# Kernel tuning notes

Measured on AMD Instinct MI355X. Metric: run time of the kernel, lower is better.

Reference implementation:

```python
import jax, jax.numpy as jnp
import numpy as np
import math
from jax import lax

KSIZE = 3
STRIDE = 1
RATE = 2
FUSE_K = 3
SCALE = 10.0
FUSE = True


def extract_image_patches(img, kernel, stride=1):
    # Faithful port of the torch helper (incl. pad_row applied to width).
    bsz, c, h, w = img.shape
    h2 = math.ceil(h / stride)
    w2 = math.ceil(w / stride)
    pad_row = (h2 - 1) * stride + kernel - h
    pad_col = (w2 - 1) * stride + kernel - w
    x = jnp.pad(img, ((0, 0), (0, 0),
                      (pad_col // 2, pad_col - pad_col // 2),
                      (pad_row // 2, pad_row - pad_row // 2)))
    H, W = x.shape[2], x.shape[3]
    nh = (H - kernel) // stride + 1
    nw = (W - kernel) // stride + 1
    parts = [x[:, :, ki:ki + (nh - 1) * stride + 1:stride,
                     kj:kj + (nw - 1) * stride + 1:stride]
             for ki in range(kernel) for kj in range(kernel)]
    p = jnp.stack(parts, axis=1)  # [b, k*k, c, nh, nw] -> flatten order (ki,kj,c)
    return p.reshape(bsz, kernel * kernel * c, nh, nw)


def setup_inputs() -> dict:
    key = jax.random.key(0)
    k1, k2 = jax.random.split(key)
    f = jax.random.normal(k1, (2, 64, 128, 128), dtype=jnp.float32)
    b = jax.random.normal(k2, (2, 64, 128, 128), dtype=jnp.float32)
    mask = jnp.zeros((2, 1, 128, 128), dtype=jnp.float32)
    return {"f": f, "b": b, "mask": mask}


def reference(f, b, mask):
    kernel = RATE * 2
    bs, cs, hs, ws = f.shape
    # raw background patches at stride=rate with kernel=2*rate
    raw_w = extract_image_patches(b, kernel, RATE * STRIDE)
    raw_w = raw_w.reshape(bs, -1, kernel, kernel, cs).transpose(0, 1, 4, 2, 3)  # [bs,L,cs,K,K]
    # nearest-neighbor downsample by rate (torch nearest: src = dst*rate)
    f_ds = f[:, :, ::RATE, ::RATE]
    b_ds = b[:, :, ::RATE, ::RATE]
    mask_ds = mask[:, :, ::RATE, ::RATE]
    ihs, iws = b_ds.shape[2], b_ds.shape[3]
    L = ihs * iws
    # ksize x ksize matching patches
    w = extract_image_patches(b_ds, KSIZE, STRIDE)
    w = w.reshape(bs, -1, KSIZE, KSIZE, cs).transpose(0, 1, 4, 2, 3)  # [bs,L,cs,3,3]
    # mask patches -> per-patch validity mm [L]
    m = extract_image_patches(mask_ds, KSIZE, STRIDE)
    m = m.reshape(bs, -1, KSIZE, KSIZE, 1).transpose(0, 2, 3, 4, 1)[0]  # [3,3,1,L]
    mm = (jnp.mean(m, axis=(0, 1, 2)) == 0.0).astype(f.dtype)  # [L]
    fuse_weight = jnp.eye(FUSE_K, dtype=f.dtype).reshape(1, 1, FUSE_K, FUSE_K)

    def per_sample(xi, wi, raw_wi):
        # xi [cs,ihs,iws], wi [L,cs,3,3], raw_wi [L,cs,K,K]
        norm = jnp.sqrt(jnp.sum(wi * wi, axis=(1, 2, 3)))
        wi_normed = wi / jnp.minimum(norm, 1e-4)[:, None, None, None]  # clamp(max=1e-4), faithful
        yi = lax.conv_general_dilated(xi[None], wi_normed, (1, 1), [(1, 1), (1, 1)])  # [1,L,ihs,iws]
        if FUSE:
            yi = yi.reshape(1, 1, ihs * iws, ihs * iws)
            yi = lax.conv_general_dilated(yi, fuse_weight, (1, 1), [(1, 1), (1, 1)])
            yi = yi.reshape(1, ihs, iws, ihs, iws).transpose(0, 2, 1, 4, 3)
            yi = yi.reshape(1, 1, ihs * iws, ihs * iws)
            yi = lax.conv_general_dilated(yi, fuse_weight, (1, 1), [(1, 1), (1, 1)])
            yi = yi.reshape(1, iws, ihs, iws, ihs).transpose(0, 2, 1, 4, 3)
        yi = yi.reshape(1, ihs, iws, iws * ihs)
        yi = jax.nn.softmax(yi * mm * SCALE, axis=3) * mm
        offset = jnp.argmax(yi, axis=3).astype(jnp.int32)
        offset = jnp.stack([offset // hs, offset % hs], axis=-1).transpose(0, 3, 1, 2)  # [1,2,ihs,iws]
        yi_t = yi.transpose(0, 3, 1, 2)  # [1,L,ihs,iws]
        # conv_transpose2d(yi_t, raw_wi, stride=rate, padding=1) via lhs dilation
        w_t = jnp.flip(raw_wi, axis=(-2, -1)).transpose(1, 0, 2, 3)  # [cs,L,K,K]
        pad = kernel - 1 - 1
        out = lax.conv_general_dilated(yi_t, w_t, (1, 1), [(pad, pad), (pad, pad)],
                                       lhs_dilation=(RATE, RATE)) / 4.0  # [1,cs,hs,ws]
        return out[0], offset[0]

    y, offsets = jax.vmap(per_sample)(f_ds, w, raw_w)
    h_add = jnp.broadcast_to(jnp.arange(ihs, dtype=offsets.dtype).reshape(1, 1, ihs, 1), (bs, 1, ihs, iws))
    w_add = jnp.broadcast_to(jnp.arange(iws, dtype=offsets.dtype).reshape(1, 1, 1, iws), (bs, 1, ihs, iws))
    offsets = offsets - jnp.concatenate([h_add, w_add], axis=1)
    return y, offsets
```

## Files before the change

### kernel.cpp

```cpp
#include <hip/hip_runtime.h>
#include <math.h>

#define NS   4096
#define KCH  576
#define CH   64
#define HF   128
#define HD   64
#define PLANE (NS*KCH)
#define IMG  (CH*HF*HF)

typedef __attribute__((ext_vector_type(8))) _Float16 half8;
typedef __attribute__((ext_vector_type(4))) float f32x4;

__device__ __forceinline__ int Tsw(int r){ return ((r & 63) << 6) | (r >> 6); }

typedef __attribute__((address_space(1))) unsigned int gu32;
typedef __attribute__((address_space(3))) unsigned int lu32;
__device__ __forceinline__ void gload16(const void* g, void* l){
  __builtin_amdgcn_global_load_lds((const gu32*)g, (lu32*)l, 16, 0, 0);
}

__global__ void k_mm(const float* __restrict__ mask, float* __restrict__ mm){
  int n = blockIdx.x * blockDim.x + threadIdx.x;
  if(n >= NS) return;
  float sum = 0.f;
  #pragma unroll
  for(int r9 = 0; r9 < 9; ++r9){
    int idx = n * 9 + r9;
    int p   = idx >> 12;
    int rem = idx & 4095;
    int y = rem >> 6, x = rem & 63;
    int ki = p / 3, kj = p % 3;
    int Y = ki + y - 1, X = kj + x - 1;
    float v = 0.f;
    if(Y >= 0 && Y < HD && X >= 0 && X < HD)
      v = mask[(2*Y) * HF + 2*X];
    sum += v;
  }
  mm[n] = ((sum / 9.0f) == 0.0f) ? 1.0f : 0.0f;
}

__global__ void k_WX(const float* __restrict__ fp, const float* __restrict__ bp,
                     _Float16* __restrict__ Wp, _Float16* __restrict__ Xp){
  int e0 = blockIdx.x * 256 + threadIdx.x;
  if(e0 < PLANE){
    int e = e0;
    int n = e / KCH, k = e - n * KCH;
    int c2 = k / 9, r9 = k - c2 * 9;
    int t = n * 9 + r9;
    int y = t & 63, ch = (t >> 6) & 63, p = t >> 12;
    int ki = p / 3, kj = p - ki * 3;
    int Y = ki + y - 1, X = kj + c2 - 1;
    float v = 0.f;
    if((unsigned)Y < 64u && (unsigned)X < 64u)
      v = bp[ch * (HF*HF) + (Y << 8) + (X << 1)];
    v *= 9.765625f;
    _Float16 h0 = (_Float16)v;
    _Float16 h1 = (_Float16)(v - (float)h0);
    Wp[e] = h0; Wp[PLANE + e] = h1;
  } else {
    int e = e0 - PLANE;
    int s = e / KCH, k = e - s * KCH;
    int c2 = k / 9, r9 = k - c2 * 9, a = r9 / 3, bb = r9 - a * 3;
    int i = s >> 6, j = s & 63;
    int Y = i + a - 1, Xc = j + bb - 1;
    float v = 0.f;
    if((unsigned)Y < 64u && (unsigned)Xc < 64u)
      v = fp[c2 * (HF*HF) + (Y << 8) + (Xc << 1)];
    v *= 1024.0f;
    _Float16 h0 = (_Float16)v;
    _Float16 h1 = (_Float16)(v - (float)h0);
    Xp[e] = h0; Xp[PLANE + e] = h1;
  }
}

#define CLUSTER(G,H,BR)                                                          \
  __builtin_amdgcn_s_setprio(1);                                                 \
  _Pragma("unroll")                                                              \
  for(int mf = 0; mf < 4; ++mf)                                                  \
    _Pragma("unroll")                                                            \
    for(int nf = 0; nf < 2; ++nf)                                                \
      _Pragma("unroll")                                                          \
      for(int ks = 0; ks < 2; ++ks)                                              \
        acc[G][mf][H][nf] = __builtin_amdgcn_mfma_f32_16x16x32_f16(              \
            Ar[mf][ks], BR[nf][ks], acc[G][mf][H][nf], 0, 0, 0);                 \
  __builtin_amdgcn_s_setprio(0);

__global__ __launch_bounds__(512, 2) void k_gemm(const _Float16* __restrict__ Wp,
                                                 const _Float16* __restrict__ Xp,
                                                 float* __restrict__ A){
  __shared__ char smem[131072];
  const int tid  = threadIdx.x;
  const int lane = tid & 63, wv = tid >> 6;
  const int wr = wv >> 2, wc = wv & 3;
  const int bid = blockIdx.x;
  const int xcd = bid & 7, slot = bid >> 3;
  const int bx = ((xcd & 3) << 2) | (slot & 3);
  const int by = ((xcd >> 2) << 3) | (slot >> 2);
  const int bn = by << 8, bs = bx << 8;

  f32x4 acc[2][4][2][2];
  #pragma unroll
  for(int g = 0; g < 2; ++g)
    #pragma unroll
    for(int mf = 0; mf < 4; ++mf)
      #pragma unroll
      for(int h = 0; h < 2; ++h)
        #pragma unroll
        for(int nf = 0; nf < 2; ++nf) acc[g][mf][h][nf] = (f32x4){0.f,0.f,0.f,0.f};

  const int srow = tid >> 3;
  const int sq8  = ((tid & 7) ^ (srow & 7)) << 3;
  const int ldso = tid << 4;

  auto stage = [&](int bufB, int t, int half){
    int term = t / 9;
    int k0 = (t - term * 9) << 6;
    const _Float16* pl;
    int rowbase, ldsbase;
    if(half == 0 || half == 3){
      pl = Wp + (size_t)(term >> 1) * PLANE;
      int g = (half == 3);
      rowbase = bn + (g << 7);
      ldsbase = bufB + (g << 14);
    } else {
      pl = Xp + (size_t)(term & 1) * PLANE;
      int h = (half == 2);
      rowbase = bs + (h << 7);
      ldsbase = bufB + 32768 + (h << 14);
    }
    const _Float16* src = pl + (size_t)(rowbase + srow) * KCH + k0 + sq8;
    gload16(src,            smem + ldsbase + ldso);
    gload16(src + 64*KCH,   smem + ldsbase + 8192 + ldso);
  };

  const int rA  = ((wr << 6) + (lane & 15)) << 7;
  const int rB  = ((wc << 5) + (lane & 15)) << 7;
  const int co0 = (((lane >> 4) ^ (lane & 7)) << 4);

  half8 Ar[4][2], B0r[2][2], B1r[2][2];
  auto readA = [&](int bufB, int g){
    const char* base = smem + bufB + (g << 14) + rA + co0;
    #pragma unroll
    for(int mf = 0; mf < 4; ++mf){
      Ar[mf][0] = *(const half8*)(base + (mf << 11));
      Ar[mf][1] = *(const half8*)(base + (mf << 11) + ((64 ^ co0) - co0));
    }
  };
  auto readB = [&](int bufB, int h, half8 (*Br)[2]){
    const char* base = smem + bufB + 32768 + (h << 14) + rB + co0;
    #pragma unroll
    for(int nf = 0; nf < 2; ++nf){
      Br[nf][0] = *(const half8*)(base + (nf << 11));
      Br[nf][1] = *(const half8*)(base + (nf << 11) + ((64 ^ co0) - co0));
    }
  };

  stage(0, 0, 0); stage(0, 0, 1); stage(0, 0, 2); stage(0, 0, 3);

  for(int t = 0; t < 27; ++t){
    const int bufB  = (t & 1) << 16;
    const int nbufB = bufB ^ 65536;
    const bool more = (t < 26);
    if(more){ stage(nbufB, t+1, 0); asm volatile("s_waitcnt vmcnt(6)" ::: "memory"); }
    else    {                       asm volatile("s_waitcnt vmcnt(4)" ::: "memory"); }
    __builtin_amdgcn_s_barrier(); asm volatile("" ::: "memory");
    readA(bufB, 0); readB(bufB, 0, B0r);
    CLUSTER(0,0,B0r)
    asm volatile("" ::: "memory"); __builtin_amdgcn_s_barrier(); asm volatile("" ::: "memory");
    if(more){ stage(nbufB, t+1, 1); asm volatile("s_waitcnt vmcnt(6)" ::: "memory"); }
    else    {                       asm volatile("s_waitcnt vmcnt(2)" ::: "memory"); }
    __builtin_amdgcn_s_barrier(); asm volatile("" ::: "memory");
    readB(bufB, 1, B1r);
    CLUSTER(0,1,B1r)
    asm volatile("" ::: "memory"); __builtin_amdgcn_s_barrier(); asm volatile("" ::: "memory");
    if(more){ stage(nbufB, t+1, 2); asm volatile("s_waitcnt vmcnt(6)" ::: "memory"); }
    else    {                       asm volatile("s_waitcnt vmcnt(0)" ::: "memory"); }
    __builtin_amdgcn_s_barrier(); asm volatile("" ::: "memory");
    readA(bufB, 1);
    CLUSTER(1,1,B1r)
    asm volatile("" ::: "memory"); __builtin_amdgcn_s_barrier(); asm volatile("" ::: "memory");
    if(more) stage(nbufB, t+1, 3);
    __builtin_amdgcn_s_barrier(); asm volatile("" ::: "memory");
    CLUSTER(1,0,B0r)
    asm volatile("" ::: "memory"); __builtin_amdgcn_s_barrier(); asm volatile("" ::: "memory");
  }

  #pragma unroll
  for(int g = 0; g < 2; ++g)
    #pragma unroll
    for(int mf = 0; mf < 4; ++mf){
      int row0 = bn + (g << 7) + (wr << 6) + (mf << 4) + ((lane >> 4) << 2);
      #pragma unroll
      for(int h = 0; h < 2; ++h)
        #pragma unroll
        for(int nf = 0; nf < 2; ++nf){
          int col = bs + (h << 7) + (wc << 5) + (nf << 4) + (lane & 15);
          #pragma unroll
          for(int r = 0; r < 4; ++r)
            A[((size_t)(row0 + r) << 12) + col] = acc[g][mf][h][nf][r];
        }
    }
}

__global__ __launch_bounds__(256) void k_f1(const float* __restrict__ A,
                                            float* __restrict__ B){
  const int n = ((blockIdx.x & 7) << 9) | (blockIdx.x >> 3);
  const int tid = threadIdx.x;
  const float* r0 = A + ((size_t)n << 12);
  const float* rm = r0 - 4096;
  const float* rp = r0 + 4096;
  const bool vm = (n >= 1), vp = (n <= 4094);
  float* Bw = B + ((size_t)n << 12);
  const float4 z4 = {0.f, 0.f, 0.f, 0.f};
  #pragma unroll
  for(int it = 0; it < 4; ++it){
    int cb = ((it << 8) + tid) << 2;
    float4 f0 = *(const float4*)(r0 + cb);
    float4 fm = vm ? *(const float4*)(rm + cb) : z4;
    float4 fp = vp ? *(const float4*)(rp + cb) : z4;
    float sm = (vm && cb > 0)    ? rm[cb - 1] : 0.f;
    float sp = (vp && cb < 4092) ? rp[cb + 4] : 0.f;
    float4 o;
    {
      float t0 = sm;           t0 += f0.x; t0 += fp.y;               o.x = t0;
      float t1 = fm.x;         t1 += f0.y; t1 += fp.z;               o.y = t1;
      float t2 = fm.y;         t2 += f0.z; t2 += fp.w;               o.z = t2;
      float t3 = fm.z;         t3 += f0.w; t3 += sp;                 o.w = t3;
    }
    *(float4*)(Bw + cb) = o;
  }
}

__global__ __launch_bounds__(256) void k_f2(const float* __restrict__ B,
                                            const float* __restrict__ mm,
                                            int* __restrict__ cnt, int* __restrict__ cand_s,
                                            float* __restrict__ cand_w,
                                            float* __restrict__ out_off){
  const int tn = ((blockIdx.x & 7) << 9) | (blockIdx.x >> 3);
  const int n  = Tsw(tn);
  const int tid = threadIdx.x;
  __shared__ float f1[256];
  __shared__ int   i1[256];
  __shared__ float s_max, s_sum;
  __shared__ int   s_cnt, s_cs[16];
  __shared__ float s_ce[16];

  const bool v2m = (tn >= 1), v2p = (tn <= 4094);
  const float* Rm = B + ((size_t)(v2m ? Tsw(tn - 1) : 0) << 12);
  const float* R0 = B + ((size_t)n << 12);
  const float* Rp = B + ((size_t)(v2p ? Tsw(tn + 1) : 0) << 12);

  const int wv = tid >> 6, ln = tid & 63;

  float z[16];
  #pragma unroll
  for(int r = 0; r < 16; ++r){
    int s = tid + (r << 8);
    int a = (r << 2) + wv;
    float tm = 0.f;
    if(v2m){
      if(a >= 1)            tm = Rm[s - 64];
      else if(ln >= 1)      tm = Rm[4031 + ln];
    }
    float t = tm;
    t += R0[s];
    float tp = 0.f;
    if(v2p){
      if(a <= 62)           tp = Rp[s + 64];
      else if(ln <= 62)     tp = Rp[ln + 1];
    }
    t += tp;
    z[r] = t;
  }

  float mmv[16];
  float lm = -3.4e38f;
  #pragma unroll
  for(int r = 0; r < 16; ++r){
    mmv[r] = mm[tid + (r << 8)];
    z[r] = z[r] * mmv[r] * 10.0f;
    lm = fmaxf(lm, z[r]);
  }
  f1[tid] = lm; __syncthreads();
  for(int st = 128; st > 0; st >>= 1){ if(tid < st) f1[tid] = fmaxf(f1[tid], f1[tid+st]); __syncthreads(); }
  if(tid == 0){ s_max = f1[0]; s_cnt = 0; }
  __syncthreads();
  float mx = s_max;

  float sum = 0.f, best = -1.0f; int bidx = 0;
  #pragma unroll
  for(int r = 0; r < 16; ++r){
    float d = z[r] - mx;
    float e = 0.f;
    if(__any(d > -20.0f)) e = expf(d);
    sum += e;
    float pe = e * mmv[r];
    int s = tid + (r << 8);
    if(pe > best){ best = pe; bidx = s; }
    if(pe > 1e-6f){
      int sl = atomicAdd(&s_cnt, 1);
      if(sl < 16){ s_cs[sl] = s; s_ce[sl] = pe; }
    }
  }
  f1[tid] = sum; __syncthreads();
  for(int st = 128; st > 0; st >>= 1){ if(tid < st) f1[tid] += f1[tid+st]; __syncthreads(); }
  if(tid == 0) s_sum = f1[0];
  __syncthreads();

  f1[tid] = best; i1[tid] = bidx; __syncthreads();
  for(int st = 128; st > 0; st >>= 1){
    if(tid < st){
      float v2 = f1[tid+st]; int j2 = i1[tid+st];
      if(v2 > f1[tid] || (v2 == f1[tid] && j2 < i1[tid])){ f1[tid] = v2; i1[tid] = j2; }
    }
    __syncthreads();
  }
  if(tid == 0){
    int sA = i1[0]; float vA = f1[0];
    int sBest = (vA > 0.0f) ? sA : 0;
    int c = min(s_cnt, 16);
    if(vA > 0.0f){
      bool found = false;
      for(int q = 0; q < c; ++q) if(s_cs[q] == sA) found = true;
      if(!found){ if(c < 16){ s_cs[c] = sA; s_ce[c] = vA; ++c; } else { s_cs[0] = sA; s_ce[0] = vA; } }
    }
    cnt[n] = c;
    float inv = 1.0f / s_sum;
    for(int q = 0; q < c; ++q){ cand_s[n*16+q] = s_cs[q]; cand_w[n*16+q] = s_ce[q] * inv; }
    out_off[n]      = (float)((sBest >> 7)  - (n >> 6));
    out_off[NS + n] = (float)((sBest & 127) - (n & 63));
  }
}

__global__ __launch_bounds__(256) void k_y(const float* __restrict__ bp,
                    const int* __restrict__ cnt, const int* __restrict__ cand_s,
                    const float* __restrict__ cand_w, float* __restrict__ outy){
  __shared__ float lv[16 * 65];
  const int sb  = blockIdx.x;
  const int oy  = sb >> 3;
  const int ox0 = (sb & 7) << 4;
  const int co  = threadIdx.x & 63, pq = threadIdx.x >> 6;
  const int kyp = oy & 1;
  const int xb  = 2 * co - 1;

  #pragma unroll
  for(int rr = 0; rr < 4; ++rr){
    const int px = (pq << 2) + rr;
    const int ox = ox0 + px;
    const int kxp = ox & 1;
    float val = 0.f;
    #pragma unroll
    for(int ia = 0; ia < 2; ++ia){
      int ky = kyp + 2*ia;
      int un = oy + ky - 2;
      if(un < 0 || un > 126) continue;
      int u = un >> 1;
      #pragma unroll
      for(int ib = 0; ib < 2; ++ib){
        int kx = kxp + 2*ib;
        int vn = ox + kx - 2;
        if(vn < 0 || vn > 126) continue;
        int v = vn >> 1;
        int n = (u << 6) | v;
        int c = cnt[n];
        int ky2 = 3 - ky, kx2 = 3 - kx;
        for(int q = 0; q < c; ++q){
          int s = cand_s[n*16 + q];
          float w = cand_w[n*16 + q];
          int p = s >> 8, ki = p >> 2, kj = p & 3, ch = (s >> 2) & 63;
          int Y = ((s & 3) << 4) + (ky2 << 2) + kx2;
          int yy = ki + 2*Y - 1;
          int xx = kj + xb;
          if(yy >= 0 && yy < HF && (unsigned)xx < (unsigned)HF)
            val += w * bp[(ch << 14) + (yy << 7) + xx];
        }
      }
    }
    lv[px * 65 + co] = val * 0.25f;
  }
  __syncthreads();
  const int pxw = threadIdx.x & 15;
  const int cw0 = threadIdx.x >> 4;
  #pragma unroll
  for(int it = 0; it < 4; ++it){
    int c2 = cw0 + (it << 4);
    outy[(c2 << 14) + (oy << 7) + ox0 + pxw] = lv[pxw * 65 + c2];
  }
}

extern "C" void kernel_launch(void* const* d_in, const int* in_sizes, int n_in,
                              void* d_out, int out_size, void* d_ws, size_t ws_size,
                              hipStream_t stream){
  const float* f    = (const float*)d_in[0];
  const float* b    = (const float*)d_in[1];
  const float* mask = (const float*)d_in[2];
  float* out = (float*)d_out;
  char* ws = (char*)d_ws;

  float*     A      = (float*)(ws);
  float*     Bf     = (float*)(ws + 67108864ull);
  _Float16*  Wp     = (_Float16*)(ws + 134217728ull);
  _Float16*  Xp     = (_Float16*)(ws + 143654912ull);
  float*     mmv    = (float*)(ws + 153092096ull);
  int*       cntv   = (int*)  (ws + 153108480ull);
  int*       cand_s = (int*)  (ws + 153124864ull);
  float*     cand_w = (float*)(ws + 153387008ull);

  k_mm<<<16, 256, 0, stream>>>(mask, mmv);

  for(int s = 0; s < 2; ++s){
    const float* fp = f + (size_t)s * IMG;
    const float* bp = b + (size_t)s * IMG;
    k_WX<<<(2*PLANE)/256, 256, 0, stream>>>(fp, bp, Wp, Xp);
    k_gemm<<<256, 512, 0, stream>>>(Wp, Xp, A);
    k_f1<<<4096, 256, 0, stream>>>(A, Bf);
    k_f2<<<4096, 256, 0, stream>>>(Bf, mmv, cntv, cand_s, cand_w,
                                   out + 2*IMG + s*2*NS);
    k_y<<<1024, 256, 0, stream>>>(bp, cntv, cand_s, cand_w,
                                  out + (size_t)s * IMG);
  }
}
```

Measured before the change: 302.1 us.

## Batch both samples into single WX and GEMM launches and trim GEMM barriers

Extends k_WX and k_gemm to handle both batch samples in one launch each, indexing by a sample id taken from the block index. The GEMM grid grows from 256 to 512 blocks so the GPU can hold two blocks per CU. Both samples' similarity matrices are kept in a larger workspace, and Bf reuses the space of the fp16 operand buffers once they are no longer needed. Inside the GEMM main loop, the stages for halves 1 and 2 are issued together and one barrier pair is removed, which reduces synchronization but raises the number of outstanding loads. The old per-sample path stays as a fallback when the workspace is too small.

```diff
diff --git a/kernel.cpp b/kernel.cpp
--- a/kernel.cpp
+++ b/kernel.cpp
@@ -40,11 +40,17 @@
   mm[n] = ((sum / 9.0f) == 0.0f) ? 1.0f : 0.0f;
 }
 
-__global__ void k_WX(const float* __restrict__ fp, const float* __restrict__ bp,
+__global__ void k_WX(const float* __restrict__ f, const float* __restrict__ b,
                      _Float16* __restrict__ Wp, _Float16* __restrict__ Xp){
   int e0 = blockIdx.x * 256 + threadIdx.x;
-  if(e0 < PLANE){
-    int e = e0;
+  int samp = e0 / (2*PLANE);
+  int ew = e0 - samp * (2*PLANE);
+  const float* fp = f + (size_t)samp * IMG;
+  const float* bp = b + (size_t)samp * IMG;
+  _Float16* Wps = Wp + (size_t)samp * (2*PLANE);
+  _Float16* Xps = Xp + (size_t)samp * (2*PLANE);
+  if(ew < PLANE){
+    int e = ew;
     int n = e / KCH, k = e - n * KCH;
     int c2 = k / 9, r9 = k - c2 * 9;
     int t = n * 9 + r9;
@@ -57,9 +63,9 @@
     v *= 9.765625f;
     _Float16 h0 = (_Float16)v;
     _Float16 h1 = (_Float16)(v - (float)h0);
-    Wp[e] = h0; Wp[PLANE + e] = h1;
+    Wps[e] = h0; Wps[PLANE + e] = h1;
   } else {
-    int e = e0 - PLANE;
+    int e = ew - PLANE;
     int s = e / KCH, k = e - s * KCH;
     int c2 = k / 9, r9 = k - c2 * 9, a = r9 / 3, bb = r9 - a * 3;
     int i = s >> 6, j = s & 63;
@@ -70,7 +76,7 @@
     v *= 1024.0f;
     _Float16 h0 = (_Float16)v;
     _Float16 h1 = (_Float16)(v - (float)h0);
-    Xp[e] = h0; Xp[PLANE + e] = h1;
+    Xps[e] = h0; Xps[PLANE + e] = h1;
   }
 }
 
@@ -93,7 +99,11 @@
   const int tid  = threadIdx.x;
   const int lane = tid & 63, wv = tid >> 6;
   const int wr = wv >> 2, wc = wv & 3;
-  const int bid = blockIdx.x;
+  const int samp = blockIdx.x >> 8;
+  const int bid  = blockIdx.x & 255;
+  const _Float16* Wps = Wp + (size_t)samp * (2*PLANE);
+  const _Float16* Xps = Xp + (size_t)samp * (2*PLANE);
+  float* As = A + (size_t)samp * NS * NS;
   const int xcd = bid & 7, slot = bid >> 3;
   const int bx = ((xcd & 3) << 2) | (slot & 3);
   const int by = ((xcd >> 2) << 3) | (slot >> 2);
@@ -119,12 +129,12 @@
     const _Float16* pl;
     int rowbase, ldsbase;
     if(half == 0 || half == 3){
-      pl = Wp + (size_t)(term >> 1) * PLANE;
+      pl = Wps + (size_t)(term >> 1) * PLANE;
       int g = (half == 3);
       rowbase = bn + (g << 7);
       ldsbase = bufB + (g << 14);
     } else {
-      pl = Xp + (size_t)(term & 1) * PLANE;
+      pl = Xps + (size_t)(term & 1) * PLANE;
       int h = (half == 2);
       rowbase = bs + (h << 7);
       ldsbase = bufB + 32768 + (h << 14);
@@ -168,20 +178,18 @@
     readA(bufB, 0); readB(bufB, 0, B0r);
     CLUSTER(0,0,B0r)
     asm volatile("" ::: "memory"); __builtin_amdgcn_s_barrier(); asm volatile("" ::: "memory");
-    if(more){ stage(nbufB, t+1, 1); asm volatile("s_waitcnt vmcnt(6)" ::: "memory"); }
-    else    {                       asm volatile("s_waitcnt vmcnt(2)" ::: "memory"); }
+    if(more){ stage(nbufB, t+1, 1); stage(nbufB, t+1, 2);
+              asm volatile("s_waitcnt vmcnt(8)" ::: "memory"); }
+    else    { asm volatile("s_waitcnt vmcnt(2)" ::: "memory"); }
     __builtin_amdgcn_s_barrier(); asm volatile("" ::: "memory");
     readB(bufB, 1, B1r);
     CLUSTER(0,1,B1r)
     asm volatile("" ::: "memory"); __builtin_amdgcn_s_barrier(); asm volatile("" ::: "memory");
-    if(more){ stage(nbufB, t+1, 2); asm volatile("s_waitcnt vmcnt(6)" ::: "memory"); }
+    if(more){ stage(nbufB, t+1, 3); asm volatile("s_waitcnt vmcnt(8)" ::: "memory"); }
     else    {                       asm volatile("s_waitcnt vmcnt(0)" ::: "memory"); }
     __builtin_amdgcn_s_barrier(); asm volatile("" ::: "memory");
     readA(bufB, 1);
     CLUSTER(1,1,B1r)
-    asm volatile("" ::: "memory"); __builtin_amdgcn_s_barrier(); asm volatile("" ::: "memory");
-    if(more) stage(nbufB, t+1, 3);
-    __builtin_amdgcn_s_barrier(); asm volatile("" ::: "memory");
     CLUSTER(1,0,B0r)
     asm volatile("" ::: "memory"); __builtin_amdgcn_s_barrier(); asm volatile("" ::: "memory");
   }
@@ -198,7 +206,7 @@
           int col = bs + (h << 7) + (wc << 5) + (nf << 4) + (lane & 15);
           #pragma unroll
           for(int r = 0; r < 4; ++r)
-            A[((size_t)(row0 + r) << 12) + col] = acc[g][mf][h][nf][r];
+            As[((size_t)(row0 + r) << 12) + col] = acc[g][mf][h][nf][r];
         }
     }
 }
@@ -398,26 +406,49 @@
   float* out = (float*)d_out;
   char* ws = (char*)d_ws;
 
-  float*     A      = (float*)(ws);
-  float*     Bf     = (float*)(ws + 67108864ull);
-  _Float16*  Wp     = (_Float16*)(ws + 134217728ull);
-  _Float16*  Xp     = (_Float16*)(ws + 143654912ull);
-  float*     mmv    = (float*)(ws + 153092096ull);
-  int*       cntv   = (int*)  (ws + 153108480ull);
-  int*       cand_s = (int*)  (ws + 153124864ull);
-  float*     cand_w = (float*)(ws + 153387008ull);
-
-  k_mm<<<16, 256, 0, stream>>>(mask, mmv);
-
-  for(int s = 0; s < 2; ++s){
-    const float* fp = f + (size_t)s * IMG;
-    const float* bp = b + (size_t)s * IMG;
-    k_WX<<<(2*PLANE)/256, 256, 0, stream>>>(fp, bp, Wp, Xp);
-    k_gemm<<<256, 512, 0, stream>>>(Wp, Xp, A);
-    k_f1<<<4096, 256, 0, stream>>>(A, Bf);
-    k_f2<<<4096, 256, 0, stream>>>(Bf, mmv, cntv, cand_s, cand_w,
-                                   out + 2*IMG + s*2*NS);
-    k_y<<<1024, 256, 0, stream>>>(bp, cntv, cand_s, cand_w,
-                                  out + (size_t)s * IMG);
-  }
-}
+  const size_t SEMI_WS = 201883648ull;
+  if(ws_size >= SEMI_WS){
+    float*    A      = (float*)(ws);
+    _Float16* Wp     = (_Float16*)(ws + 134217728ull);
+    _Float16* Xp     = (_Float16*)(ws + 153092096ull);
+    float*    Bf     = (float*)(ws + 134217728ull);
+    float*    mmv    = (float*)(ws + 201326592ull);
+    int*      cntv   = (int*)  (ws + 201342976ull);
+    int*      cand_s = (int*)  (ws + 201359360ull);
+    float*    cand_w = (float*)(ws + 201621504ull);
+
+    k_mm<<<16, 256, 0, stream>>>(mask, mmv);
+    k_WX<<<(4*PLANE)/256, 256, 0, stream>>>(f, b, Wp, Xp);
+    k_gemm<<<512, 512, 0, stream>>>(Wp, Xp, A);
+    for(int s = 0; s < 2; ++s){
+      const float* bp = b + (size_t)s * IMG;
+      k_f1<<<4096, 256, 0, stream>>>(A + (size_t)s * NS * NS, Bf);
+      k_f2<<<4096, 256, 0, stream>>>(Bf, mmv, cntv, cand_s, cand_w,
+                                     out + 2*IMG + s*2*NS);
+      k_y<<<1024, 256, 0, stream>>>(bp, cntv, cand_s, cand_w,
+                                    out + (size_t)s * IMG);
+    }
+  } else {
+    float*     A      = (float*)(ws);
+    float*     Bf     = (float*)(ws + 67108864ull);
+    _Float16*  Wp     = (_Float16*)(ws + 134217728ull);
+    _Float16*  Xp     = (_Float16*)(ws + 143654912ull);
+    float*     mmv    = (float*)(ws + 153092096ull);
+    int*       cntv   = (int*)  (ws + 153108480ull);
+    int*       cand_s = (int*)  (ws + 153124864ull);
+    float*     cand_w = (float*)(ws + 153387008ull);
+
+    k_mm<<<16, 256, 0, stream>>>(mask, mmv);
+    for(int s = 0; s < 2; ++s){
+      const float* fp = f + (size_t)s * IMG;
+      const float* bp = b + (size_t)s * IMG;
+      k_WX<<<(2*PLANE)/256, 256, 0, stream>>>(fp, bp, Wp, Xp);
+      k_gemm<<<256, 512, 0, stream>>>(Wp, Xp, A);
+      k_f1<<<4096, 256, 0, stream>>>(A, Bf);
+      k_f2<<<4096, 256, 0, stream>>>(Bf, mmv, cntv, cand_s, cand_w,
+                                     out + 2*IMG + s*2*NS);
+      k_y<<<1024, 256, 0, stream>>>(bp, cntv, cand_s, cand_w,
+                                    out + (size_t)s * IMG);
+    }
+  }
+}
```

New measurement: 300.2 us. Within noise of the previous version (-0.6%).
